# Kernel optimization log

Hardware: AMD Instinct MI355X
Metric: run time of the kernel (lower is better)

## Reference

```python
import jax, jax.numpy as jnp
import numpy as np

FP8_E4M3_MAX = 448.0  # max finite value of float8_e4m3fn
ACT_SCALE = 2.0       # self.scale in the torch module
WEIGHT_SCALE = 2.0    # self.weight_scale in the torch module


def qdq_fp8(x, scale):
    """quantize_affine_float8 (clamp + cast to e4m3fn) then dequantize back to f32."""
    q = jnp.clip(x / scale, -FP8_E4M3_MAX, FP8_E4M3_MAX).astype(jnp.float8_e4m3fn)
    return q.astype(jnp.float32) * scale


def setup_inputs() -> dict:
    key = jax.random.key(0)
    k1, k2, k3 = jax.random.split(key, 3)
    x = jax.random.normal(k1, (32, 128, 56, 56), dtype=jnp.float32)
    # weight is stored in fp8 in the torch module; round-trip through fp8 so the
    # f32 tensor holds exactly representable fp8 values.
    w = jax.random.normal(k2, (256, 128, 3, 3), dtype=jnp.float32)
    w = w.astype(jnp.float8_e4m3fn).astype(jnp.float32)
    b = jax.random.normal(k3, (256,), dtype=jnp.float32)
    return {"input": x, "weight": w, "bias": b}


def reference(input, weight, bias):
    # dequantize fp8 weight: cast-to-f32 already done in setup, apply scale
    w = weight * WEIGHT_SCALE
    # quantize + dequantize the activation through fp8 e4m3
    dq_input = qdq_fp8(input, ACT_SCALE)
    out = jax.lax.conv_general_dilated(
        dq_input, w,
        window_strides=(1, 1),
        padding=[(1, 1), (1, 1)],
        lhs_dilation=(1, 1),
        rhs_dilation=(1, 1),  # dilation=1
        dimension_numbers=("NCHW", "OIHW", "NCHW"),
        feature_group_count=1,
    )
    return out + bias[None, :, None, None]
```

## Files before the change

### kernel.cpp

```cpp
#include <hip/hip_runtime.h>
#include <cstdint>


#define NB   32
#define CIN  128
#define HW   56
#define KOUT 256

#define ACT_BYTES (32u * 56u * 56u * 128u)
#define WT_OFF    ACT_BYTES
#define WT_BYTES  (9u * 256u * 128u)
#define ZP_OFF    (WT_OFF + WT_BYTES)

typedef float        f32x4 __attribute__((ext_vector_type(4)));
typedef unsigned int u32x4 __attribute__((ext_vector_type(4)));

__device__ __forceinline__ unsigned int pack2_fp8(float a, float b) {
  a = fminf(fmaxf(a, -448.f), 448.f);
  b = fminf(fmaxf(b, -448.f), 448.f);
  return (unsigned int)__builtin_amdgcn_cvt_pk_fp8_f32(a, b, 0, false);
}

__global__ __launch_bounds__(256) void qdq_pack(const float* __restrict__ X,
                                                unsigned char* __restrict__ act) {
  const int nh = blockIdx.x;
  const int n = nh / HW, h = nh - n * HW;
  const float* xb = X + (size_t)n * (CIN * HW * HW) + h * HW;
  unsigned char* ob = act + (size_t)nh * (HW * CIN);

  for (int i = 0; i < 2; ++i) {
    int item = threadIdx.x + i * 256;
    if (item >= HW * 8) break;
    int w = item % HW, cg = item / HW;
    unsigned int dw[4];
#pragma unroll
    for (int jj = 0; jj < 4; ++jj) {
      int c0 = cg * 16 + jj * 4;
      float v0 = xb[(c0 + 0) * 3136 + w] * 0.5f;
      float v1 = xb[(c0 + 1) * 3136 + w] * 0.5f;
      float v2 = xb[(c0 + 2) * 3136 + w] * 0.5f;
      float v3 = xb[(c0 + 3) * 3136 + w] * 0.5f;
      unsigned int lo = pack2_fp8(v0, v1) & 0xffffu;
      unsigned int hi = pack2_fp8(v2, v3) & 0xffffu;
      dw[jj] = lo | (hi << 16);
    }
    u32x4 v = {dw[0], dw[1], dw[2], dw[3]};
    *(u32x4*)(ob + w * CIN + cg * 16) = v;
  }
}

__global__ __launch_bounds__(256) void pack_weight(const float* __restrict__ W,
                                                   unsigned char* __restrict__ wt,
                                                   unsigned int* __restrict__ zp) {
  if (blockIdx.x == 0 && threadIdx.x < 32) zp[threadIdx.x] = 0u;
  int gid = blockIdx.x * 256 + threadIdx.x;
  int o = gid * 4;
  if (o >= (int)WT_BYTES) return;
  int rs = o >> 15;
  int rem = o & 32767;
  int k  = rem >> 7;
  int c0 = rem & 127;
  float v0 = W[k * 1152 + (c0 + 0) * 9 + rs];
  float v1 = W[k * 1152 + (c0 + 1) * 9 + rs];
  float v2 = W[k * 1152 + (c0 + 2) * 9 + rs];
  float v3 = W[k * 1152 + (c0 + 3) * 9 + rs];
  unsigned int dw = (pack2_fp8(v0, v1) & 0xffffu) | (pack2_fp8(v2, v3) << 16);
  *(unsigned int*)(wt + o) = dw;
}

__device__ __forceinline__ void g2l16(const void* g, void* l) {
  __builtin_amdgcn_global_load_lds((const __attribute__((address_space(1))) void*)g,
                                   (__attribute__((address_space(3))) void*)l,
                                   16, 0, 0);
}

__global__ __launch_bounds__(256) void conv_mfma(const unsigned char* __restrict__ act,
                                                 const unsigned char* __restrict__ wt,
                                                 const unsigned char* __restrict__ zp,
                                                 const float* __restrict__ bias,
                                                 float* __restrict__ out) {
  __shared__ __align__(16) unsigned char lds[32768];
  const int tid  = threadIdx.x;
  const int lane = tid & 63;
  const int wid  = tid >> 6;
  const int wr   = wid >> 1, wc = wid & 1;
  const int bm   = blockIdx.x << 7;
  const int bn   = blockIdx.y << 7;

  const int srow   = tid >> 3;
  const int sphys  = (tid & 7) << 4;
  const int schunk = ((tid & 7) ^ (srow & 7)) << 4;

  int an_[4], ah_[4], aw_[4];
#pragma unroll
  for (int q = 0; q < 4; ++q) {
    int m = bm + srow + 32 * q;
    int n = m / 3136;
    int hw = m - n * 3136;
    int h = hw / 56;
    an_[q] = n; ah_[q] = h; aw_[q] = hw - h * 56;
  }

  const f32x4 zero = {0.f, 0.f, 0.f, 0.f};
  f32x4 acc[4][4];
#pragma unroll
  for (int i = 0; i < 4; ++i)
#pragma unroll
    for (int j = 0; j < 4; ++j) acc[i][j] = zero;

  for (int rs = 0; rs < 9; ++rs) {
    const int r = rs / 3, s = rs - 3 * (rs / 3);
    const unsigned char* wseg = wt + rs * (KOUT * CIN);

#pragma unroll
    for (int q = 0; q < 4; ++q) {
      int hi = ah_[q] + r - 1;
      int wi = aw_[q] + s - 1;
      bool ok = ((unsigned)hi < 56u) && ((unsigned)wi < 56u);
      const unsigned char* src =
          ok ? act + (((an_[q] * 56 + hi) * 56 + wi) << 7) + schunk : zp + schunk;
      g2l16(src, &lds[((srow + 32 * q) << 7) + sphys]);
    }
#pragma unroll
    for (int q = 0; q < 4; ++q) {
      int kl = srow + 32 * q;
      g2l16(wseg + ((bn + kl) << 7) + schunk, &lds[16384 + (kl << 7) + sphys]);
    }
    __syncthreads();

    const int kgrp = (lane >> 4) << 3;
    const int xa   = (lane & 7) << 4;
#pragma unroll
    for (int kk = 0; kk < 4; ++kk) {
      const int kb = kk * 32 + kgrp;
      long av[4], bv[4];
#pragma unroll
      for (int mi = 0; mi < 4; ++mi) {
        int row = (wr << 6) + (mi << 4) + (lane & 15);
        av[mi] = *(const long*)(&lds[(row << 7) + (kb ^ xa)]);
      }
#pragma unroll
      for (int ni = 0; ni < 4; ++ni) {
        int col = (wc << 6) + (ni << 4) + (lane & 15);
        bv[ni] = *(const long*)(&lds[16384 + (col << 7) + (kb ^ xa)]);
      }
#pragma unroll
      for (int mi = 0; mi < 4; ++mi)
#pragma unroll
        for (int ni = 0; ni < 4; ++ni)
          acc[mi][ni] = __builtin_amdgcn_mfma_f32_16x16x32_fp8_fp8(
              av[mi], bv[ni], acc[mi][ni], 0, 0, 0);
    }
    __syncthreads();
  }

#pragma unroll
  for (int ni = 0; ni < 4; ++ni) {
    int k = bn + (wc << 6) + (ni << 4) + (lane & 15);
    float bvv = bias[k];
#pragma unroll
    for (int mi = 0; mi < 4; ++mi) {
      int m = bm + (wr << 6) + (mi << 4) + ((lane >> 4) << 2);
      int n = m / 3136;
      int hw = m - n * 3136;
      f32x4 v = acc[mi][ni];
      v = v * 4.0f + bvv;
      *(f32x4*)(out + (size_t)(n * KOUT + k) * 3136 + hw) = v;
    }
  }
}

extern "C" void kernel_launch(void* const* d_in, const int* in_sizes, int n_in,
                              void* d_out, int out_size, void* d_ws, size_t ws_size,
                              hipStream_t stream) {
  const float* X = (const float*)d_in[0];
  const float* W = (const float*)d_in[1];
  const float* B = (const float*)d_in[2];
  float* out = (float*)d_out;

  unsigned char* act = (unsigned char*)d_ws;
  unsigned char* wtb = act + WT_OFF;
  unsigned char* zp  = act + ZP_OFF;

  hipLaunchKernelGGL(qdq_pack,    dim3(NB * HW), dim3(256), 0, stream, X, act);
  hipLaunchKernelGGL(pack_weight, dim3(288),     dim3(256), 0, stream, W, wtb,
                     (unsigned int*)zp);
  hipLaunchKernelGGL(conv_mfma,   dim3(784, 2),  dim3(256), 0, stream, act, wtb, zp, B,
                     out);
}
```

Before: 82.77 us.

## Stage activation halo once in LDS and double-buffer weight tiles across filter taps

Instead of reloading a 128-row activation tile from global memory for each of the 9 filter taps, the conv kernel now loads a contiguous 244-pixel halo window into LDS (most of it up front, the rest in two later increments). Each tap reads from this window at a shifted offset and masks out-of-bounds pixels in registers, which replaces the zero-page pointer trick. Weight tiles are double-buffered so the next tap's weights are fetched while the current tap computes. The intent is to cut global/L2 traffic for activations and overlap weight loads with MFMA work, at the cost of more LDS (about 63KB per block), which may lower occupancy.

New measurement: 88.62 us. 7.1% more time.

```diff
diff --git a/kernel.cpp b/kernel.cpp
--- a/kernel.cpp
+++ b/kernel.cpp
@@ -6,11 +6,11 @@
 #define CIN  128
 #define HW   56
 #define KOUT 256
+#define MTOT (32 * 56 * 56)
 
 #define ACT_BYTES (32u * 56u * 56u * 128u)
 #define WT_OFF    ACT_BYTES
 #define WT_BYTES  (9u * 256u * 128u)
-#define ZP_OFF    (WT_OFF + WT_BYTES)
 
 typedef float        f32x4 __attribute__((ext_vector_type(4)));
 typedef unsigned int u32x4 __attribute__((ext_vector_type(4)));
@@ -50,9 +50,7 @@
 }
 
 __global__ __launch_bounds__(256) void pack_weight(const float* __restrict__ W,
-                                                   unsigned char* __restrict__ wt,
-                                                   unsigned int* __restrict__ zp) {
-  if (blockIdx.x == 0 && threadIdx.x < 32) zp[threadIdx.x] = 0u;
+                                                   unsigned char* __restrict__ wt) {
   int gid = blockIdx.x * 256 + threadIdx.x;
   int o = gid * 4;
   if (o >= (int)WT_BYTES) return;
@@ -76,30 +74,46 @@
 
 __global__ __launch_bounds__(256) void conv_mfma(const unsigned char* __restrict__ act,
                                                  const unsigned char* __restrict__ wt,
-                                                 const unsigned char* __restrict__ zp,
                                                  const float* __restrict__ bias,
                                                  float* __restrict__ out) {
-  __shared__ __align__(16) unsigned char lds[32768];
+  __shared__ __align__(16) unsigned char ldsA[244 * 128];
+  __shared__ __align__(16) unsigned char ldsB[2][16384];
   const int tid  = threadIdx.x;
   const int lane = tid & 63;
   const int wid  = tid >> 6;
   const int wr   = wid >> 1, wc = wid & 1;
   const int bm   = blockIdx.x << 7;
   const int bn   = blockIdx.y << 7;
-
-  const int srow   = tid >> 3;
-  const int sphys  = (tid & 7) << 4;
-  const int schunk = ((tid & 7) ^ (srow & 7)) << 4;
-
-  int an_[4], ah_[4], aw_[4];
+  const int pbase = bm - 57;
+
+  int h_[4], w_[4];
+#pragma unroll
+  for (int mi = 0; mi < 4; ++mi) {
+    int m = bm + (wr << 6) + (mi << 4) + (lane & 15);
+    int hw = m % 3136;
+    h_[mi] = hw / 56;
+    w_[mi] = hw - 56 * (hw / 56);
+  }
+
+#pragma unroll
+  for (int q = 0; q < 5; ++q) {
+    int item = tid + (q << 8);
+    if (item < 1040) {
+      int slot = item >> 3, chunk = item & 7;
+      int p = pbase + slot;
+      p = p < 0 ? 0 : (p > MTOT - 1 ? MTOT - 1 : p);
+      g2l16(act + ((size_t)p << 7) + ((chunk ^ (slot & 7)) << 4),
+            ldsA + (item << 4));
+    }
+  }
 #pragma unroll
   for (int q = 0; q < 4; ++q) {
-    int m = bm + srow + 32 * q;
-    int n = m / 3136;
-    int hw = m - n * 3136;
-    int h = hw / 56;
-    an_[q] = n; ah_[q] = h; aw_[q] = hw - h * 56;
-  }
+    int item = tid + (q << 8);
+    int krow = item >> 3, chunk = item & 7;
+    g2l16(wt + ((bn + krow) << 7) + ((chunk ^ (krow & 7)) << 4),
+          ldsB[0] + (item << 4));
+  }
+  __syncthreads();
 
   const f32x4 zero = {0.f, 0.f, 0.f, 0.f};
   f32x4 acc[4][4];
@@ -109,40 +123,59 @@
     for (int j = 0; j < 4; ++j) acc[i][j] = zero;
 
   for (int rs = 0; rs < 9; ++rs) {
-    const int r = rs / 3, s = rs - 3 * (rs / 3);
-    const unsigned char* wseg = wt + rs * (KOUT * CIN);
-
-#pragma unroll
-    for (int q = 0; q < 4; ++q) {
-      int hi = ah_[q] + r - 1;
-      int wi = aw_[q] + s - 1;
-      bool ok = ((unsigned)hi < 56u) && ((unsigned)wi < 56u);
-      const unsigned char* src =
-          ok ? act + (((an_[q] * 56 + hi) * 56 + wi) << 7) + schunk : zp + schunk;
-      g2l16(src, &lds[((srow + 32 * q) << 7) + sphys]);
-    }
-#pragma unroll
-    for (int q = 0; q < 4; ++q) {
-      int kl = srow + 32 * q;
-      g2l16(wseg + ((bn + kl) << 7) + schunk, &lds[16384 + (kl << 7) + sphys]);
-    }
-    __syncthreads();
-
+    const int r = rs / 3;
+    const int s = rs - 3 * r;
+    const int cur = rs & 1;
+
+    if (rs < 8) {
+      const unsigned char* wseg = wt + (rs + 1) * (KOUT * CIN);
+#pragma unroll
+      for (int q = 0; q < 4; ++q) {
+        int item = tid + (q << 8);
+        int krow = item >> 3, chunk = item & 7;
+        g2l16(wseg + ((bn + krow) << 7) + ((chunk ^ (krow & 7)) << 4),
+              ldsB[cur ^ 1] + (item << 4));
+      }
+    }
+    if (s == 0 && r < 2) {
+      const int slotbase = 130 + 56 * r;
+#pragma unroll
+      for (int q = 0; q < 2; ++q) {
+        int item = tid + (q << 8);
+        if (item < 448) {
+          int slot = slotbase + (item >> 3), chunk = item & 7;
+          int p = pbase + slot;
+          p = p < 0 ? 0 : (p > MTOT - 1 ? MTOT - 1 : p);
+          g2l16(act + ((size_t)p << 7) + ((chunk ^ (slot & 7)) << 4),
+                ldsA + (slot << 7) + (chunk << 4));
+        }
+      }
+    }
+
+    const int slotw = 56 * r + s + (wr << 6) + (lane & 15);
+    int slot_[4], vmask[4];
+#pragma unroll
+    for (int mi = 0; mi < 4; ++mi) {
+      slot_[mi] = slotw + (mi << 4);
+      vmask[mi] = (int)(((unsigned)(h_[mi] + r - 1) < 56u) &
+                        ((unsigned)(w_[mi] + s - 1) < 56u));
+    }
+    const unsigned char* bseg = ldsB[cur];
     const int kgrp = (lane >> 4) << 3;
-    const int xa   = (lane & 7) << 4;
 #pragma unroll
     for (int kk = 0; kk < 4; ++kk) {
-      const int kb = kk * 32 + kgrp;
+      const int kb = (kk << 5) + kgrp;
       long av[4], bv[4];
 #pragma unroll
       for (int mi = 0; mi < 4; ++mi) {
-        int row = (wr << 6) + (mi << 4) + (lane & 15);
-        av[mi] = *(const long*)(&lds[(row << 7) + (kb ^ xa)]);
+        int sl = slot_[mi];
+        long v = *(const long*)(ldsA + (sl << 7) + (kb ^ ((sl & 7) << 4)));
+        av[mi] = vmask[mi] ? v : 0L;
       }
 #pragma unroll
       for (int ni = 0; ni < 4; ++ni) {
         int col = (wc << 6) + (ni << 4) + (lane & 15);
-        bv[ni] = *(const long*)(&lds[16384 + (col << 7) + (kb ^ xa)]);
+        bv[ni] = *(const long*)(bseg + (col << 7) + (kb ^ ((col & 7) << 4)));
       }
 #pragma unroll
       for (int mi = 0; mi < 4; ++mi)
@@ -151,6 +184,7 @@
           acc[mi][ni] = __builtin_amdgcn_mfma_f32_16x16x32_fp8_fp8(
               av[mi], bv[ni], acc[mi][ni], 0, 0, 0);
     }
+
     __syncthreads();
   }
 
@@ -180,11 +214,9 @@
 
   unsigned char* act = (unsigned char*)d_ws;
   unsigned char* wtb = act + WT_OFF;
-  unsigned char* zp  = act + ZP_OFF;
 
   hipLaunchKernelGGL(qdq_pack,    dim3(NB * HW), dim3(256), 0, stream, X, act);
-  hipLaunchKernelGGL(pack_weight, dim3(288),     dim3(256), 0, stream, W, wtb,
-                     (unsigned int*)zp);
-  hipLaunchKernelGGL(conv_mfma,   dim3(784, 2),  dim3(256), 0, stream, act, wtb, zp, B,
+  hipLaunchKernelGGL(pack_weight, dim3(288),     dim3(256), 0, stream, W, wtb);
+  hipLaunchKernelGGL(conv_mfma,   dim3(784, 2),  dim3(256), 0, stream, act, wtb, B,
                      out);
 }
```

## Triple-buffer conv mainloop with 256x128 tiles and register-side padding masks

Applied to the files above, without the earlier changes.

Restructures the MFMA conv kernel into a triple-buffered LDS pipeline. The reduction is split into 18 half-channel steps, so the next stages' global-to-LDS loads overlap the current MFMAs, using manual vmcnt waits and a single barrier per step. Blocks grow to 512 threads covering a 256x128 output tile, with a swizzled block order. Padding is handled by clamping the source row and zeroing out-of-bounds A fragments in registers, which removes the zero-page buffer. The larger LDS footprint lowers occupancy, and the hand-written waitcnt and scheduling barriers add fragility.

New measurement: 98.85 us. 1.19x slower.

```diff
diff --git a/kernel.cpp b/kernel.cpp
--- a/kernel.cpp
+++ b/kernel.cpp
@@ -6,11 +6,11 @@
 #define CIN  128
 #define HW   56
 #define KOUT 256
+#define MTOT (32 * 56 * 56)
 
 #define ACT_BYTES (32u * 56u * 56u * 128u)
 #define WT_OFF    ACT_BYTES
 #define WT_BYTES  (9u * 256u * 128u)
-#define ZP_OFF    (WT_OFF + WT_BYTES)
 
 typedef float        f32x4 __attribute__((ext_vector_type(4)));
 typedef unsigned int u32x4 __attribute__((ext_vector_type(4)));
@@ -50,9 +50,7 @@
 }
 
 __global__ __launch_bounds__(256) void pack_weight(const float* __restrict__ W,
-                                                   unsigned char* __restrict__ wt,
-                                                   unsigned int* __restrict__ zp) {
-  if (blockIdx.x == 0 && threadIdx.x < 32) zp[threadIdx.x] = 0u;
+                                                   unsigned char* __restrict__ wt) {
   int gid = blockIdx.x * 256 + threadIdx.x;
   int o = gid * 4;
   if (o >= (int)WT_BYTES) return;
@@ -74,32 +72,60 @@
                                    16, 0, 0);
 }
 
-__global__ __launch_bounds__(256) void conv_mfma(const unsigned char* __restrict__ act,
-                                                 const unsigned char* __restrict__ wt,
-                                                 const unsigned char* __restrict__ zp,
-                                                 const float* __restrict__ bias,
-                                                 float* __restrict__ out) {
-  __shared__ __align__(16) unsigned char lds[32768];
+__global__ __launch_bounds__(512, 4) void conv_mfma(const unsigned char* __restrict__ act,
+                                                    const unsigned char* __restrict__ wt,
+                                                    const float* __restrict__ bias,
+                                                    float* __restrict__ out) {
+  __shared__ __align__(16) unsigned char ldsA[3][16384];
+  __shared__ __align__(16) unsigned char ldsB[3][8192];
+
   const int tid  = threadIdx.x;
   const int lane = tid & 63;
   const int wid  = tid >> 6;
   const int wr   = wid >> 1, wc = wid & 1;
-  const int bm   = blockIdx.x << 7;
-  const int bn   = blockIdx.y << 7;
-
-  const int srow   = tid >> 3;
-  const int sphys  = (tid & 7) << 4;
-  const int schunk = ((tid & 7) ^ (srow & 7)) << 4;
-
-  int an_[4], ah_[4], aw_[4];
-#pragma unroll
-  for (int q = 0; q < 4; ++q) {
-    int m = bm + srow + 32 * q;
-    int n = m / 3136;
-    int hw = m - n * 3136;
-    int h = hw / 56;
-    an_[q] = n; ah_[q] = h; aw_[q] = hw - h * 56;
-  }
+
+  const int idx  = (int)blockIdx.x;
+  const int nidx = (idx & 7) * 98 + (idx >> 3);
+  const int bmi  = nidx % 392, bni = nidx / 392;
+  const int bm   = bmi << 8;
+  const int bn   = bni << 7;
+
+  int h_[4], w_[4];
+#pragma unroll
+  for (int mi = 0; mi < 4; ++mi) {
+    int m = bm + (wr << 6) + (mi << 4) + (lane & 15);
+    int hw = m % 3136;
+    h_[mi] = hw / 56;
+    w_[mi] = hw - 56 * (hw / 56);
+  }
+
+  auto stage = [&](int tt) {
+    const int rs2 = tt >> 1;
+    const int chalf = (tt & 1) << 6;
+    const int r = rs2 / 3, s = rs2 - 3 * r;
+    const int off = 56 * (r - 1) + (s - 1);
+    unsigned char* bA = ldsA[tt % 3];
+    unsigned char* bB = ldsB[tt % 3];
+    const unsigned char* wseg = wt + (rs2 << 15) + chalf;
+#pragma unroll
+    for (int q = 0; q < 2; ++q) {
+      int c = tid + (q << 9);
+      int rp = c >> 3, slot = c & 7;
+      int sp = slot ^ (rp & 7);
+      int row = (rp << 1) + (sp >> 2);
+      int kb = (sp & 3) << 4;
+      int p = bm + row + off;
+      p = p < 0 ? 0 : (p > MTOT - 1 ? MTOT - 1 : p);
+      g2l16(act + ((size_t)p << 7) + chalf + kb, bA + (c << 4));
+    }
+    {
+      int rp = tid >> 3, slot = tid & 7;
+      int sp = slot ^ (rp & 7);
+      int krow = (rp << 1) + (sp >> 2);
+      int kb = (sp & 3) << 4;
+      g2l16(wseg + ((size_t)(bn + krow) << 7) + kb, bB + (tid << 4));
+    }
+  };
 
   const f32x4 zero = {0.f, 0.f, 0.f, 0.f};
   f32x4 acc[4][4];
@@ -108,42 +134,48 @@
 #pragma unroll
     for (int j = 0; j < 4; ++j) acc[i][j] = zero;
 
-  for (int rs = 0; rs < 9; ++rs) {
-    const int r = rs / 3, s = rs - 3 * (rs / 3);
-    const unsigned char* wseg = wt + rs * (KOUT * CIN);
-
-#pragma unroll
-    for (int q = 0; q < 4; ++q) {
-      int hi = ah_[q] + r - 1;
-      int wi = aw_[q] + s - 1;
-      bool ok = ((unsigned)hi < 56u) && ((unsigned)wi < 56u);
-      const unsigned char* src =
-          ok ? act + (((an_[q] * 56 + hi) * 56 + wi) << 7) + schunk : zp + schunk;
-      g2l16(src, &lds[((srow + 32 * q) << 7) + sphys]);
-    }
-#pragma unroll
-    for (int q = 0; q < 4; ++q) {
-      int kl = srow + 32 * q;
-      g2l16(wseg + ((bn + kl) << 7) + schunk, &lds[16384 + (kl << 7) + sphys]);
-    }
-    __syncthreads();
-
-    const int kgrp = (lane >> 4) << 3;
-    const int xa   = (lane & 7) << 4;
-#pragma unroll
-    for (int kk = 0; kk < 4; ++kk) {
-      const int kb = kk * 32 + kgrp;
+  auto rdA = [&](const unsigned char* buf, int row, int b) -> long {
+    int rp = row >> 1;
+    int pb = ((row & 1) << 6) + b;
+    return *(const long*)(buf + (rp << 7) + ((((pb >> 4) ^ (rp & 7)) << 4) | (pb & 15)));
+  };
+
+  stage(0);
+  stage(1);
+
+  for (int t = 0; t < 18; ++t) {
+    if (t < 17) {
+      asm volatile("s_waitcnt vmcnt(3)" ::: "memory");
+    } else {
+      asm volatile("s_waitcnt vmcnt(0)" ::: "memory");
+    }
+    __builtin_amdgcn_sched_barrier(0);
+    __builtin_amdgcn_s_barrier();
+    __builtin_amdgcn_sched_barrier(0);
+    if (t < 16) stage(t + 2);
+
+    const int rs2 = t >> 1;
+    const int r = rs2 / 3, s = rs2 - 3 * r;
+    const unsigned char* bA = ldsA[t % 3];
+    const unsigned char* bB = ldsB[t % 3];
+    int vmask[4];
+#pragma unroll
+    for (int mi = 0; mi < 4; ++mi)
+      vmask[mi] = (int)(((unsigned)(h_[mi] + r - 1) < 56u) &
+                        ((unsigned)(w_[mi] + s - 1) < 56u));
+    __builtin_amdgcn_s_setprio(1);
+#pragma unroll
+    for (int kk = 0; kk < 2; ++kk) {
+      const int kbf = (kk << 5) + ((lane >> 4) << 3);
       long av[4], bv[4];
 #pragma unroll
       for (int mi = 0; mi < 4; ++mi) {
-        int row = (wr << 6) + (mi << 4) + (lane & 15);
-        av[mi] = *(const long*)(&lds[(row << 7) + (kb ^ xa)]);
+        long v = rdA(bA, (wr << 6) + (mi << 4) + (lane & 15), kbf);
+        av[mi] = vmask[mi] ? v : 0L;
       }
 #pragma unroll
-      for (int ni = 0; ni < 4; ++ni) {
-        int col = (wc << 6) + (ni << 4) + (lane & 15);
-        bv[ni] = *(const long*)(&lds[16384 + (col << 7) + (kb ^ xa)]);
-      }
+      for (int ni = 0; ni < 4; ++ni)
+        bv[ni] = rdA(bB, (wc << 6) + (ni << 4) + (lane & 15), kbf);
 #pragma unroll
       for (int mi = 0; mi < 4; ++mi)
 #pragma unroll
@@ -151,7 +183,7 @@
           acc[mi][ni] = __builtin_amdgcn_mfma_f32_16x16x32_fp8_fp8(
               av[mi], bv[ni], acc[mi][ni], 0, 0, 0);
     }
-    __syncthreads();
+    __builtin_amdgcn_s_setprio(0);
   }
 
 #pragma unroll
@@ -180,11 +212,9 @@
 
   unsigned char* act = (unsigned char*)d_ws;
   unsigned char* wtb = act + WT_OFF;
-  unsigned char* zp  = act + ZP_OFF;
 
   hipLaunchKernelGGL(qdq_pack,    dim3(NB * HW), dim3(256), 0, stream, X, act);
-  hipLaunchKernelGGL(pack_weight, dim3(288),     dim3(256), 0, stream, W, wtb,
-                     (unsigned int*)zp);
-  hipLaunchKernelGGL(conv_mfma,   dim3(784, 2),  dim3(256), 0, stream, act, wtb, zp, B,
+  hipLaunchKernelGGL(pack_weight, dim3(288),     dim3(256), 0, stream, W, wtb);
+  hipLaunchKernelGGL(conv_mfma,   dim3(784),     dim3(512), 0, stream, act, wtb, B,
                      out);
 }
```

## Load activation fragments directly from global and double-buffer weight tiles in LDS

Applied to the files above, without the earlier changes.

Activation MFMA operands are now read straight from global memory into registers, one 8-byte fragment per lane, instead of being staged through LDS. The first k-slice of the next filter tap is prefetched into registers. Weight tiles are double-buffered in LDS so the next tap's copy overlaps the current tap's MFMAs. This removes the LDS round trip and one barrier's worth of stall for activations, at the cost of uncoalesced 8-byte global loads, more live registers, and a fully unrolled loop.

Result: slower. 158.0 us (+90.9%).

```diff
diff --git a/kernel.cpp b/kernel.cpp
--- a/kernel.cpp
+++ b/kernel.cpp
@@ -6,6 +6,7 @@
 #define CIN  128
 #define HW   56
 #define KOUT 256
+#define MTOT (32 * 56 * 56)
 
 #define ACT_BYTES (32u * 56u * 56u * 128u)
 #define WT_OFF    ACT_BYTES
@@ -79,7 +80,7 @@
                                                  const unsigned char* __restrict__ zp,
                                                  const float* __restrict__ bias,
                                                  float* __restrict__ out) {
-  __shared__ __align__(16) unsigned char lds[32768];
+  __shared__ __align__(16) unsigned char ldsB[2][16384];
   const int tid  = threadIdx.x;
   const int lane = tid & 63;
   const int wid  = tid >> 6;
@@ -91,15 +92,31 @@
   const int sphys  = (tid & 7) << 4;
   const int schunk = ((tid & 7) ^ (srow & 7)) << 4;
 
-  int an_[4], ah_[4], aw_[4];
-#pragma unroll
-  for (int q = 0; q < 4; ++q) {
-    int m = bm + srow + 32 * q;
+  int fn[4], fh[4], fw[4];
+#pragma unroll
+  for (int mi = 0; mi < 4; ++mi) {
+    int m = bm + (wr << 6) + (mi << 4) + (lane & 15);
     int n = m / 3136;
     int hw = m - n * 3136;
     int h = hw / 56;
-    an_[q] = n; ah_[q] = h; aw_[q] = hw - h * 56;
-  }
+    fn[mi] = n; fh[mi] = h; fw[mi] = hw - h * 56;
+  }
+  const int laneoff = (lane >> 4) << 3;
+
+  auto stageB = [&](unsigned char* buf, int rs) {
+    const unsigned char* wseg = wt + rs * (KOUT * CIN);
+#pragma unroll
+    for (int q = 0; q < 4; ++q) {
+      int kl = srow + 32 * q;
+      g2l16(wseg + ((bn + kl) << 7) + schunk, buf + (kl << 7) + sphys);
+    }
+  };
+  auto abase = [&](int mi, int r, int s) -> const unsigned char* {
+    int hi = fh[mi] + r - 1;
+    int wi = fw[mi] + s - 1;
+    bool ok = ((unsigned)hi < 56u) && ((unsigned)wi < 56u);
+    return (ok ? act + ((size_t)((fn[mi] * 56 + hi) * 56 + wi) << 7) : zp) + laneoff;
+  };
 
   const f32x4 zero = {0.f, 0.f, 0.f, 0.f};
   f32x4 acc[4][4];
@@ -108,49 +125,55 @@
 #pragma unroll
     for (int j = 0; j < 4; ++j) acc[i][j] = zero;
 
+  stageB(ldsB[0], 0);
+  long av0[4];
+#pragma unroll
+  for (int mi = 0; mi < 4; ++mi) av0[mi] = *(const long*)(abase(mi, 0, 0));
+  __syncthreads();
+
+#pragma unroll
   for (int rs = 0; rs < 9; ++rs) {
-    const int r = rs / 3, s = rs - 3 * (rs / 3);
-    const unsigned char* wseg = wt + rs * (KOUT * CIN);
-
-#pragma unroll
-    for (int q = 0; q < 4; ++q) {
-      int hi = ah_[q] + r - 1;
-      int wi = aw_[q] + s - 1;
-      bool ok = ((unsigned)hi < 56u) && ((unsigned)wi < 56u);
-      const unsigned char* src =
-          ok ? act + (((an_[q] * 56 + hi) * 56 + wi) << 7) + schunk : zp + schunk;
-      g2l16(src, &lds[((srow + 32 * q) << 7) + sphys]);
-    }
-#pragma unroll
-    for (int q = 0; q < 4; ++q) {
-      int kl = srow + 32 * q;
-      g2l16(wseg + ((bn + kl) << 7) + schunk, &lds[16384 + (kl << 7) + sphys]);
-    }
-    __syncthreads();
-
-    const int kgrp = (lane >> 4) << 3;
-    const int xa   = (lane & 7) << 4;
-#pragma unroll
-    for (int kk = 0; kk < 4; ++kk) {
-      const int kb = kk * 32 + kgrp;
-      long av[4], bv[4];
-#pragma unroll
-      for (int mi = 0; mi < 4; ++mi) {
-        int row = (wr << 6) + (mi << 4) + (lane & 15);
-        av[mi] = *(const long*)(&lds[(row << 7) + (kb ^ xa)]);
-      }
+    const int r = rs / 3, s = rs - 3 * r;
+    if (rs < 8) stageB(ldsB[(rs + 1) & 1], rs + 1);
+
+    const unsigned char* bbuf = ldsB[rs & 1];
+    long bv[4][4];
+#pragma unroll
+    for (int kk = 0; kk < 4; ++kk)
 #pragma unroll
       for (int ni = 0; ni < 4; ++ni) {
         int col = (wc << 6) + (ni << 4) + (lane & 15);
-        bv[ni] = *(const long*)(&lds[16384 + (col << 7) + (kb ^ xa)]);
+        bv[kk][ni] = *(const long*)(
+            bbuf + (col << 7) + (((kk << 5) + laneoff) ^ ((col & 7) << 4)));
       }
+
+    const unsigned char* ab[4];
+#pragma unroll
+    for (int mi = 0; mi < 4; ++mi) ab[mi] = abase(mi, r, s);
+    long av[4][4];
+#pragma unroll
+    for (int mi = 0; mi < 4; ++mi) av[0][mi] = av0[mi];
+#pragma unroll
+    for (int kk = 1; kk < 4; ++kk)
+#pragma unroll
+      for (int mi = 0; mi < 4; ++mi)
+        av[kk][mi] = *(const long*)(ab[mi] + (kk << 5));
+
+    if (rs < 8) {
+      const int rn = (rs + 1) / 3, sn = (rs + 1) - 3 * ((rs + 1) / 3);
+#pragma unroll
+      for (int mi = 0; mi < 4; ++mi) av0[mi] = *(const long*)(abase(mi, rn, sn));
+    }
+
+#pragma unroll
+    for (int kk = 0; kk < 4; ++kk)
 #pragma unroll
       for (int mi = 0; mi < 4; ++mi)
 #pragma unroll
         for (int ni = 0; ni < 4; ++ni)
           acc[mi][ni] = __builtin_amdgcn_mfma_f32_16x16x32_fp8_fp8(
-              av[mi], bv[ni], acc[mi][ni], 0, 0, 0);
-    }
+              av[kk][mi], bv[kk][ni], acc[mi][ni], 0, 0, 0);
+
     __syncthreads();
   }
 
```
